# Kernel tuning notes

Hardware: AMD Instinct MI355X
Metric: run time of the kernel (lower is better)

The kernel has to match this reference:

```python
import jax, jax.numpy as jnp
import numpy as np

HC = 128   # hidden_channels
H = 8      # num_heads
D = HC // H  # projected_channels per head
N = 50000
M = 400000


def setup_inputs() -> dict:
    key = jax.random.key(0)
    ks = jax.random.split(key, 9)
    s = 1.0 / np.sqrt(HC)
    return {
        "query": jax.random.normal(ks[0], (N, HC), jnp.float32),
        "key": jax.random.normal(ks[1], (N, HC), jnp.float32),
        "query_index": jax.random.randint(ks[2], (M,), 0, N),
        "key_index": jax.random.randint(ks[3], (M,), 0, N),
        "paired_repr": jax.random.normal(ks[4], (M, HC), jnp.float32),
        "Wq": jax.random.uniform(ks[5], (HC, D * H), jnp.float32, -s, s),
        "Wkv": jax.random.uniform(ks[6], (HC, 2 * D * H), jnp.float32, -s, s),
        "Wb": jax.random.uniform(ks[7], (HC, 2 * D * H), jnp.float32, -s, s),
        "Wo": jax.random.uniform(ks[8], (D * H, HC), jnp.float32, -s, s),
    }


def reference(query, key, query_index, key_index, paired_repr, Wq, Wkv, Wb, Wo):
    n = query.shape[0]
    m = paired_repr.shape[0]
    # projections
    q = (query @ Wq).reshape(n, D, H)
    kv = key @ Wkv                              # (N, 2*D*H)
    k = kv[:, : D * H].reshape(n, D, H)
    v = kv[:, D * H :].reshape(n, D, H)
    # gather per interaction
    q_e = q[query_index]                        # (M, D, H)
    k_e = k[key_index]
    v_e = v[key_index]
    b = paired_repr @ Wb                        # (M, 2*D*H)
    bias_mul = b[:, : D * H].reshape(m, D, H)
    bias_add = b[:, D * H :].reshape(m, D, H)
    # bias-modulated dot-product logits per head
    logit = jnp.sum(q_e * (k_e * (1.0 + bias_mul) + bias_add), axis=1)  # (M, H)
    # segment softmax over query_index groups
    seg_max = jax.ops.segment_max(logit, query_index, num_segments=n)
    ex = jnp.exp(logit - seg_max[query_index])
    denom = jax.ops.segment_sum(ex, query_index, num_segments=n)
    attn = ex / denom[query_index]              # (M, H)
    # scatter-add weighted values
    agg = jax.ops.segment_sum(attn[:, None, :] * v_e, query_index, num_segments=n)  # (N, D, H)
    result = agg.reshape(n, D * H) @ Wo         # (N, HC)
    return result, logit
```

## Files before the change

### kernel.cpp

```cpp
#include <hip/hip_runtime.h>


#define HC 128
#define NH 8
#define ND 16

typedef __attribute__((ext_vector_type(8))) short bf16x8;
typedef __attribute__((ext_vector_type(4))) float f32x4;
typedef __attribute__((ext_vector_type(4))) unsigned int u32x4;

static __device__ __forceinline__ unsigned short f2bf(float f) {
  unsigned u = __float_as_uint(f);
  unsigned r = 0x7fffu + ((u >> 16) & 1u);
  return (unsigned short)((u + r) >> 16);
}
static __device__ __forceinline__ float bf2f(unsigned short h) {
  return __uint_as_float(((unsigned)h) << 16);
}

__global__ __launch_bounds__(256) void convert_wb_kernel(
    const float* __restrict__ Wb, unsigned short* __restrict__ WbTp) {
  int idx = blockIdx.x * 256 + threadIdx.x;
  int kt = idx >> 13, j = (idx >> 5) & 255, kk = idx & 31;
  WbTp[idx] = f2bf(Wb[(kt * 32 + kk) * 256 + j]);
}

__global__ __launch_bounds__(256) void count_kernel(const int* __restrict__ qidx,
                                                    int* __restrict__ cnt, int M) {
  int m = blockIdx.x * 256 + threadIdx.x;
  if (m < M) atomicAdd(&cnt[qidx[m]], 1);
}

__global__ __launch_bounds__(1024) void scan_kernel(int* __restrict__ cnt,
                                                    int* __restrict__ off, int N) {
  __shared__ int partial[1024];
  const int tid = threadIdx.x;
  const int K = (N + 1023) / 1024;
  const int lo = tid * K;
  int s = 0;
  for (int i = 0; i < K; ++i) {
    int idx = lo + i;
    if (idx < N) s += cnt[idx];
  }
  partial[tid] = s;
  __syncthreads();
  for (int d = 1; d < 1024; d <<= 1) {
    int t = (tid >= d) ? partial[tid - d] : 0;
    __syncthreads();
    partial[tid] += t;
    __syncthreads();
  }
  int run = partial[tid] - s;
  for (int i = 0; i < K; ++i) {
    int idx = lo + i;
    if (idx < N) {
      off[idx] = run;
      run += cnt[idx];
      cnt[idx] = 0;
    }
  }
  if (tid == 1023) off[N] = run;
}

__global__ __launch_bounds__(256) void fill_kernel(const int* __restrict__ qidx,
                                                   int* __restrict__ cursor,
                                                   const int* __restrict__ off,
                                                   int* __restrict__ el, int M) {
  int m = blockIdx.x * 256 + threadIdx.x;
  if (m < M) {
    int qi = qidx[m];
    int pos = atomicAdd(&cursor[qi], 1);
    el[off[qi] + pos] = m;
  }
}

__global__ __launch_bounds__(256) void proj_kernel(
    const float* __restrict__ query, const float* __restrict__ key,
    const float* __restrict__ Wq, const float* __restrict__ Wkv,
    float* __restrict__ qp, float* __restrict__ kp, float* __restrict__ vp, int N) {
  __shared__ float q_lds[16][HC];
  __shared__ float k_lds[16][HC];
  const int tid = threadIdx.x;
  const int base = blockIdx.x * 16;
  for (int i = tid; i < 16 * HC; i += 256) {
    int e = i >> 7, c = i & 127;
    int node = base + e;
    float qv = 0.f, kv = 0.f;
    if (node < N) {
      qv = query[(size_t)node * HC + c];
      kv = key[(size_t)node * HC + c];
    }
    q_lds[e][c] = qv;
    k_lds[e][c] = kv;
  }
  __syncthreads();
  {
    int j = tid & 127, e0 = tid >> 7;
    float acc[8] = {0.f, 0.f, 0.f, 0.f, 0.f, 0.f, 0.f, 0.f};
    for (int c = 0; c < HC; ++c) {
      float w = Wq[c * 128 + j];
#pragma unroll
      for (int r = 0; r < 8; ++r) acc[r] += q_lds[e0 + 2 * r][c] * w;
    }
#pragma unroll
    for (int r = 0; r < 8; ++r) {
      int node = base + e0 + 2 * r;
      if (node < N) qp[(size_t)node * 128 + j] = acc[r];
    }
  }
  {
    float acc[16];
#pragma unroll
    for (int e = 0; e < 16; ++e) acc[e] = 0.f;
    for (int c = 0; c < HC; ++c) {
      float w = Wkv[c * 256 + tid];
#pragma unroll
      for (int e = 0; e < 16; ++e) acc[e] += k_lds[e][c] * w;
    }
    float* dst = (tid < 128) ? kp : vp;
    int j = tid & 127;
#pragma unroll
    for (int e = 0; e < 16; ++e) {
      int node = base + e;
      if (node < N) dst[(size_t)node * 128 + j] = acc[e];
    }
  }
}

#define BLS 264
__global__ __launch_bounds__(256) void edge_logit_mfma(
    const float* __restrict__ pr, const unsigned short* __restrict__ WbTp,
    const float* __restrict__ qp, const float* __restrict__ kp,
    const int* __restrict__ qidx, const int* __restrict__ kidx,
    float* __restrict__ out_logit, int M) {
  __shared__ unsigned char lds[64 * BLS * 2];
  const int tid = threadIdx.x;
  const int base = blockIdx.x * 64;

#pragma unroll
  for (int i = 0; i < 4; ++i) {
    int q = tid + 256 * i;
    int row = q >> 4, cr = q & 15;
    int m = base + row;
    float4 p0 = {0.f, 0.f, 0.f, 0.f}, p1 = p0;
    if (m < M) {
      const float4* src = (const float4*)(pr + (size_t)m * HC + cr * 8);
      p0 = src[0];
      p1 = src[1];
    }
    unsigned v0 = (unsigned)f2bf(p0.x) | ((unsigned)f2bf(p0.y) << 16);
    unsigned v1 = (unsigned)f2bf(p0.z) | ((unsigned)f2bf(p0.w) << 16);
    unsigned v2 = (unsigned)f2bf(p1.x) | ((unsigned)f2bf(p1.y) << 16);
    unsigned v3 = (unsigned)f2bf(p1.z) | ((unsigned)f2bf(p1.w) << 16);
    u32x4 pk = {v0, v1, v2, v3};
    int byte = row * 256 + ((cr * 16) ^ ((row & 7) << 4));
    *(u32x4*)(lds + byte) = pk;
  }
  __syncthreads();

  const int lane = tid & 63, w = tid >> 6;
  const int arow = w * 16 + (lane & 15);
  bf16x8 a[4];
#pragma unroll
  for (int kt = 0; kt < 4; ++kt) {
    int byte = arow * 256 + ((kt * 64 + ((lane >> 4) * 16)) ^ ((arow & 7) << 4));
    a[kt] = *(const bf16x8*)(lds + byte);
  }
  __syncthreads();

  f32x4 acc[16];
#pragma unroll
  for (int n = 0; n < 16; ++n) acc[n] = (f32x4){0.f, 0.f, 0.f, 0.f};
#pragma unroll
  for (int kt = 0; kt < 4; ++kt) {
#pragma unroll
    for (int n = 0; n < 16; ++n) {
      bf16x8 b = *(const bf16x8*)(WbTp + kt * 8192 + (n * 16 + (lane & 15)) * 32 +
                                  (lane >> 4) * 8);
      acc[n] = __builtin_amdgcn_mfma_f32_16x16x32_bf16(a[kt], b, acc[n], 0, 0, 0);
    }
  }

  unsigned short* bl = (unsigned short*)lds;
  {
    int col = (lane & 15);
    int r0 = w * 16 + (lane >> 4) * 4;
#pragma unroll
    for (int n = 0; n < 16; ++n) {
#pragma unroll
      for (int r = 0; r < 4; ++r) bl[(r0 + r) * BLS + n * 16 + col] = f2bf(acc[n][r]);
    }
  }
  __syncthreads();

#pragma unroll
  for (int rep = 0; rep < 2; ++rep) {
    int unit = rep * 256 + tid;
    int e = unit >> 3, h = unit & 7;
    int m = base + e;
    if (m < M) {
      int qi = qidx[m], ki = kidx[m];
      const float* qrow = qp + (size_t)qi * HC;
      const float* krow = kp + (size_t)ki * HC;
      float s = 0.f;
#pragma unroll
      for (int d = 0; d < ND; ++d) {
        int c = d * 8 + h;
        float bm = bf2f(bl[e * BLS + c]);
        float ba = bf2f(bl[e * BLS + c + 128]);
        s += qrow[c] * (krow[c] * (1.f + bm) + ba);
      }
      out_logit[(size_t)m * 8 + h] = s;
    }
  }
}

__global__ __launch_bounds__(128) void node_agg_kernel(
    const float* __restrict__ vp, const float* __restrict__ logit,
    const int* __restrict__ kidx, const int* __restrict__ off,
    const int* __restrict__ el, float* __restrict__ agg, int N) {
  const int n = blockIdx.x;
  const int c = threadIdx.x;
  const int h = c & 7;
  const int s = off[n], e = off[n + 1];
  float mx = -1e30f;
  for (int i = s; i < e; ++i) {
    int m = el[i];
    mx = fmaxf(mx, logit[(size_t)m * 8 + h]);
  }
  float acc = 0.f, dsum = 0.f;
  for (int i = s; i < e; ++i) {
    int m = el[i];
    float ex = __expf(logit[(size_t)m * 8 + h] - mx);
    acc += ex * vp[(size_t)kidx[m] * HC + c];
    dsum += ex;
  }
  agg[(size_t)n * HC + c] = (e > s) ? acc / dsum : 0.f;
}

__global__ __launch_bounds__(256) void out_kernel(
    const float* __restrict__ agg, const float* __restrict__ Wo,
    float* __restrict__ out, int N) {
  __shared__ float a_lds[16][HC];
  const int tid = threadIdx.x;
  const int base = blockIdx.x * 16;
  for (int i = tid; i < 16 * HC; i += 256) {
    int e = i >> 7, c = i & 127;
    int node = base + e;
    a_lds[e][c] = (node < N) ? agg[(size_t)node * 128 + c] : 0.f;
  }
  __syncthreads();
  int j = tid & 127, e0 = tid >> 7;
  float acc[8] = {0.f, 0.f, 0.f, 0.f, 0.f, 0.f, 0.f, 0.f};
  for (int c = 0; c < HC; ++c) {
    float w = Wo[c * 128 + j];
#pragma unroll
    for (int r = 0; r < 8; ++r) acc[r] += a_lds[e0 + 2 * r][c] * w;
  }
#pragma unroll
  for (int r = 0; r < 8; ++r) {
    int node = base + e0 + 2 * r;
    if (node < N) out[(size_t)node * 128 + j] = acc[r];
  }
}

extern "C" void kernel_launch(void* const* d_in, const int* in_sizes, int n_in,
                              void* d_out, int out_size, void* d_ws, size_t ws_size,
                              hipStream_t stream) {
  const float* query = (const float*)d_in[0];
  const float* key   = (const float*)d_in[1];
  const int*   qidx  = (const int*)d_in[2];
  const int*   kidx  = (const int*)d_in[3];
  const float* pr    = (const float*)d_in[4];
  const float* Wq    = (const float*)d_in[5];
  const float* Wkv   = (const float*)d_in[6];
  const float* Wb    = (const float*)d_in[7];
  const float* Wo    = (const float*)d_in[8];

  const int N = in_sizes[0] / HC;
  const int M = in_sizes[2];

  float* out_result = (float*)d_out;
  float* out_logit  = (float*)d_out + (size_t)N * HC;

  float* qp  = (float*)d_ws;
  float* kp  = qp + (size_t)N * HC;
  float* vp  = kp + (size_t)N * HC;
  float* agg = vp + (size_t)N * HC;
  unsigned short* WbTp = (unsigned short*)(agg + (size_t)N * HC);
  int* cnt = (int*)(WbTp + 4 * 256 * 32);
  int* off = cnt + N;
  int* el  = off + (N + 1);

  hipMemsetAsync(cnt, 0, (size_t)N * sizeof(int), stream);
  count_kernel<<<(M + 255) / 256, 256, 0, stream>>>(qidx, cnt, M);
  scan_kernel<<<1, 1024, 0, stream>>>(cnt, off, N);
  convert_wb_kernel<<<128, 256, 0, stream>>>(Wb, WbTp);
  proj_kernel<<<(N + 15) / 16, 256, 0, stream>>>(query, key, Wq, Wkv, qp, kp, vp, N);
  edge_logit_mfma<<<(M + 63) / 64, 256, 0, stream>>>(pr, WbTp, qp, kp, qidx, kidx,
                                                     out_logit, M);
  fill_kernel<<<(M + 255) / 256, 256, 0, stream>>>(qidx, cnt, off, el, M);
  node_agg_kernel<<<N, 128, 0, stream>>>(vp, out_logit, kidx, off, el, agg, N);
  out_kernel<<<(N + 15) / 16, 256, 0, stream>>>(agg, Wo, out_result, N);
}
```

Baseline: 925.1 us.

## Move projections and output GEMM to bf16 MFMA and use online-softmax aggregation

Replaces the scalar FP32 projection and output GEMMs with bf16 MFMA kernels, using pre-converted packed weights. Stores q/k/v and the aggregate in bf16 to halve gather bandwidth. Rewrites edge logits so each wave reduces one edge's heads with shuffles. Node aggregation now runs one wave per node with a single-pass online softmax, reading precomputed (edge, key) pairs from the CSR list so kidx is no longer looked up per edge. Lower precision in the intermediates adds rounding error.

```diff
diff --git a/kernel.cpp b/kernel.cpp
--- a/kernel.cpp
+++ b/kernel.cpp
@@ -3,7 +3,6 @@
 
 #define HC 128
 #define NH 8
-#define ND 16
 
 typedef __attribute__((ext_vector_type(8))) short bf16x8;
 typedef __attribute__((ext_vector_type(4))) float f32x4;
@@ -17,12 +16,24 @@
 static __device__ __forceinline__ float bf2f(unsigned short h) {
   return __uint_as_float(((unsigned)h) << 16);
 }
-
-__global__ __launch_bounds__(256) void convert_wb_kernel(
-    const float* __restrict__ Wb, unsigned short* __restrict__ WbTp) {
+static __device__ __forceinline__ float bflo(unsigned w) { return __uint_as_float(w << 16); }
+static __device__ __forceinline__ float bfhi(unsigned w) { return __uint_as_float(w & 0xffff0000u); }
+
+__global__ __launch_bounds__(256) void convert_w_kernel(
+    const float* __restrict__ Wq, const float* __restrict__ Wkv,
+    const float* __restrict__ Wb, const float* __restrict__ Wo,
+    unsigned short* __restrict__ P) {
   int idx = blockIdx.x * 256 + threadIdx.x;
-  int kt = idx >> 13, j = (idx >> 5) & 255, kk = idx & 31;
-  WbTp[idx] = f2bf(Wb[(kt * 32 + kk) * 256 + j]);
+  const float* W;
+  int cols, local;
+  if (idx < 16384) { W = Wq; cols = 128; local = idx; }
+  else if (idx < 49152) { W = Wkv; cols = 256; local = idx - 16384; }
+  else if (idx < 81920) { W = Wb; cols = 256; local = idx - 49152; }
+  else { W = Wo; cols = 128; local = idx - 81920; }
+  int kt = local / (cols * 32);
+  int j = (local / 32) % cols;
+  int kk = local & 31;
+  P[idx] = f2bf(W[(kt * 32 + kk) * cols + j]);
 }
 
 __global__ __launch_bounds__(256) void count_kernel(const int* __restrict__ qidx,
@@ -63,102 +74,160 @@
 }
 
 __global__ __launch_bounds__(256) void fill_kernel(const int* __restrict__ qidx,
+                                                   const int* __restrict__ kidx,
                                                    int* __restrict__ cursor,
                                                    const int* __restrict__ off,
-                                                   int* __restrict__ el, int M) {
+                                                   int2* __restrict__ el2, int M) {
   int m = blockIdx.x * 256 + threadIdx.x;
   if (m < M) {
     int qi = qidx[m];
     int pos = atomicAdd(&cursor[qi], 1);
-    el[off[qi] + pos] = m;
-  }
-}
-
-__global__ __launch_bounds__(256) void proj_kernel(
+    int2 v; v.x = m; v.y = kidx[m];
+    el2[off[qi] + pos] = v;
+  }
+}
+
+__global__ __launch_bounds__(256) void proj_mfma(
     const float* __restrict__ query, const float* __restrict__ key,
-    const float* __restrict__ Wq, const float* __restrict__ Wkv,
-    float* __restrict__ qp, float* __restrict__ kp, float* __restrict__ vp, int N) {
-  __shared__ float q_lds[16][HC];
-  __shared__ float k_lds[16][HC];
+    const unsigned short* __restrict__ WqP, const unsigned short* __restrict__ WkvP,
+    unsigned short* __restrict__ qpb, unsigned short* __restrict__ kpb,
+    unsigned short* __restrict__ vpb, int N) {
+  __shared__ unsigned char lds[32768];
   const int tid = threadIdx.x;
-  const int base = blockIdx.x * 16;
-  for (int i = tid; i < 16 * HC; i += 256) {
-    int e = i >> 7, c = i & 127;
-    int node = base + e;
-    float qv = 0.f, kv = 0.f;
+  const int base = blockIdx.x * 64;
+  const int lane = tid & 63, w = tid >> 6;
+
+#pragma unroll
+  for (int i = 0; i < 4; ++i) {
+    int q = tid + 256 * i;
+    int row = q >> 4, cr = q & 15;
+    int node = base + row;
+    float4 a0 = {0.f,0.f,0.f,0.f}, a1 = a0, b0 = a0, b1 = a0;
     if (node < N) {
-      qv = query[(size_t)node * HC + c];
-      kv = key[(size_t)node * HC + c];
-    }
-    q_lds[e][c] = qv;
-    k_lds[e][c] = kv;
-  }
-  __syncthreads();
+      const float4* sq = (const float4*)(query + (size_t)node * HC + cr * 8);
+      const float4* sk = (const float4*)(key + (size_t)node * HC + cr * 8);
+      a0 = sq[0]; a1 = sq[1]; b0 = sk[0]; b1 = sk[1];
+    }
+    int byte = row * 256 + ((cr << 4) ^ ((row & 7) << 4));
+    u32x4 pa = {(unsigned)f2bf(a0.x) | ((unsigned)f2bf(a0.y) << 16),
+                (unsigned)f2bf(a0.z) | ((unsigned)f2bf(a0.w) << 16),
+                (unsigned)f2bf(a1.x) | ((unsigned)f2bf(a1.y) << 16),
+                (unsigned)f2bf(a1.z) | ((unsigned)f2bf(a1.w) << 16)};
+    u32x4 pb = {(unsigned)f2bf(b0.x) | ((unsigned)f2bf(b0.y) << 16),
+                (unsigned)f2bf(b0.z) | ((unsigned)f2bf(b0.w) << 16),
+                (unsigned)f2bf(b1.x) | ((unsigned)f2bf(b1.y) << 16),
+                (unsigned)f2bf(b1.z) | ((unsigned)f2bf(b1.w) << 16)};
+    *(u32x4*)(lds + byte) = pa;
+    *(u32x4*)(lds + 16384 + byte) = pb;
+  }
+  __syncthreads();
+
+  const int arow = w * 16 + (lane & 15);
+  bf16x8 aq[4], ak[4];
+#pragma unroll
+  for (int kt = 0; kt < 4; ++kt) {
+    int byte = arow * 256 + ((kt * 64 + ((lane >> 4) * 16)) ^ ((arow & 7) << 4));
+    aq[kt] = *(const bf16x8*)(lds + byte);
+    ak[kt] = *(const bf16x8*)(lds + 16384 + byte);
+  }
+  __syncthreads();
+
+  unsigned short* stg = (unsigned short*)lds;
+
   {
-    int j = tid & 127, e0 = tid >> 7;
-    float acc[8] = {0.f, 0.f, 0.f, 0.f, 0.f, 0.f, 0.f, 0.f};
-    for (int c = 0; c < HC; ++c) {
-      float w = Wq[c * 128 + j];
-#pragma unroll
-      for (int r = 0; r < 8; ++r) acc[r] += q_lds[e0 + 2 * r][c] * w;
-    }
-#pragma unroll
-    for (int r = 0; r < 8; ++r) {
-      int node = base + e0 + 2 * r;
-      if (node < N) qp[(size_t)node * 128 + j] = acc[r];
-    }
-  }
+    f32x4 acc[8];
+#pragma unroll
+    for (int n = 0; n < 8; ++n) acc[n] = (f32x4){0.f,0.f,0.f,0.f};
+#pragma unroll
+    for (int kt = 0; kt < 4; ++kt)
+#pragma unroll
+      for (int n = 0; n < 8; ++n) {
+        bf16x8 b = *(const bf16x8*)(WqP + kt * 4096 + (n * 16 + (lane & 15)) * 32 + (lane >> 4) * 8);
+        acc[n] = __builtin_amdgcn_mfma_f32_16x16x32_bf16(aq[kt], b, acc[n], 0, 0, 0);
+      }
+    int lc = lane & 15, r0 = w * 16 + (lane >> 4) * 4;
+#pragma unroll
+    for (int n = 0; n < 8; ++n)
+#pragma unroll
+      for (int r = 0; r < 4; ++r) {
+        int row = r0 + r, col = n * 16 + lc;
+        int byte = row * 256 + ((((col >> 3) ^ (row & 7)) << 4)) + (col & 7) * 2;
+        *(unsigned short*)((unsigned char*)stg + byte) = f2bf(acc[n][r]);
+      }
+#pragma unroll
+    for (int it = 0; it < 4; ++it) {
+      int q = it * 64 + lane;
+      int row = w * 16 + (q >> 4), ch = q & 15;
+      int node = base + row;
+      u32x4 v = *(const u32x4*)(lds + row * 256 + ((ch ^ (row & 7)) << 4));
+      if (node < N) *(u32x4*)(qpb + (size_t)node * HC + ch * 8) = v;
+    }
+  }
+
   {
-    float acc[16];
-#pragma unroll
-    for (int e = 0; e < 16; ++e) acc[e] = 0.f;
-    for (int c = 0; c < HC; ++c) {
-      float w = Wkv[c * 256 + tid];
-#pragma unroll
-      for (int e = 0; e < 16; ++e) acc[e] += k_lds[e][c] * w;
-    }
-    float* dst = (tid < 128) ? kp : vp;
-    int j = tid & 127;
-#pragma unroll
-    for (int e = 0; e < 16; ++e) {
-      int node = base + e;
-      if (node < N) dst[(size_t)node * 128 + j] = acc[e];
+    f32x4 acc[16];
+#pragma unroll
+    for (int n = 0; n < 16; ++n) acc[n] = (f32x4){0.f,0.f,0.f,0.f};
+#pragma unroll
+    for (int kt = 0; kt < 4; ++kt)
+#pragma unroll
+      for (int n = 0; n < 16; ++n) {
+        bf16x8 b = *(const bf16x8*)(WkvP + kt * 8192 + (n * 16 + (lane & 15)) * 32 + (lane >> 4) * 8);
+        acc[n] = __builtin_amdgcn_mfma_f32_16x16x32_bf16(ak[kt], b, acc[n], 0, 0, 0);
+      }
+    int lc = lane & 15, r0 = w * 16 + (lane >> 4) * 4;
+#pragma unroll
+    for (int half = 0; half < 2; ++half) {
+#pragma unroll
+      for (int n = 0; n < 8; ++n)
+#pragma unroll
+        for (int r = 0; r < 4; ++r) {
+          int row = r0 + r, col = n * 16 + lc;
+          int byte = row * 256 + ((((col >> 3) ^ (row & 7)) << 4)) + (col & 7) * 2;
+          *(unsigned short*)((unsigned char*)stg + byte) = f2bf(acc[half * 8 + n][r]);
+        }
+      unsigned short* dst = half ? vpb : kpb;
+#pragma unroll
+      for (int it = 0; it < 4; ++it) {
+        int q = it * 64 + lane;
+        int row = w * 16 + (q >> 4), ch = q & 15;
+        int node = base + row;
+        u32x4 v = *(const u32x4*)(lds + row * 256 + ((ch ^ (row & 7)) << 4));
+        if (node < N) *(u32x4*)(dst + (size_t)node * HC + ch * 8) = v;
+      }
     }
   }
 }
 
 #define BLS 264
 __global__ __launch_bounds__(256) void edge_logit_mfma(
-    const float* __restrict__ pr, const unsigned short* __restrict__ WbTp,
-    const float* __restrict__ qp, const float* __restrict__ kp,
+    const float* __restrict__ pr, const unsigned short* __restrict__ WbP,
+    const unsigned short* __restrict__ qpb, const unsigned short* __restrict__ kpb,
     const int* __restrict__ qidx, const int* __restrict__ kidx,
     float* __restrict__ out_logit, int M) {
   __shared__ unsigned char lds[64 * BLS * 2];
   const int tid = threadIdx.x;
   const int base = blockIdx.x * 64;
+  const int lane = tid & 63, w = tid >> 6;
 
 #pragma unroll
   for (int i = 0; i < 4; ++i) {
     int q = tid + 256 * i;
     int row = q >> 4, cr = q & 15;
     int m = base + row;
-    float4 p0 = {0.f, 0.f, 0.f, 0.f}, p1 = p0;
+    float4 p0 = {0.f,0.f,0.f,0.f}, p1 = p0;
     if (m < M) {
       const float4* src = (const float4*)(pr + (size_t)m * HC + cr * 8);
-      p0 = src[0];
-      p1 = src[1];
-    }
-    unsigned v0 = (unsigned)f2bf(p0.x) | ((unsigned)f2bf(p0.y) << 16);
-    unsigned v1 = (unsigned)f2bf(p0.z) | ((unsigned)f2bf(p0.w) << 16);
-    unsigned v2 = (unsigned)f2bf(p1.x) | ((unsigned)f2bf(p1.y) << 16);
-    unsigned v3 = (unsigned)f2bf(p1.z) | ((unsigned)f2bf(p1.w) << 16);
-    u32x4 pk = {v0, v1, v2, v3};
-    int byte = row * 256 + ((cr * 16) ^ ((row & 7) << 4));
-    *(u32x4*)(lds + byte) = pk;
-  }
-  __syncthreads();
-
-  const int lane = tid & 63, w = tid >> 6;
+      p0 = src[0]; p1 = src[1];
+    }
+    u32x4 pk = {(unsigned)f2bf(p0.x) | ((unsigned)f2bf(p0.y) << 16),
+                (unsigned)f2bf(p0.z) | ((unsigned)f2bf(p0.w) << 16),
+                (unsigned)f2bf(p1.x) | ((unsigned)f2bf(p1.y) << 16),
+                (unsigned)f2bf(p1.z) | ((unsigned)f2bf(p1.w) << 16)};
+    *(u32x4*)(lds + row * 256 + ((cr << 4) ^ ((row & 7) << 4))) = pk;
+  }
+  __syncthreads();
+
   const int arow = w * 16 + (lane & 15);
   bf16x8 a[4];
 #pragma unroll
@@ -170,97 +239,136 @@
 
   f32x4 acc[16];
 #pragma unroll
-  for (int n = 0; n < 16; ++n) acc[n] = (f32x4){0.f, 0.f, 0.f, 0.f};
-#pragma unroll
-  for (int kt = 0; kt < 4; ++kt) {
+  for (int n = 0; n < 16; ++n) acc[n] = (f32x4){0.f,0.f,0.f,0.f};
+#pragma unroll
+  for (int kt = 0; kt < 4; ++kt)
 #pragma unroll
     for (int n = 0; n < 16; ++n) {
-      bf16x8 b = *(const bf16x8*)(WbTp + kt * 8192 + (n * 16 + (lane & 15)) * 32 +
-                                  (lane >> 4) * 8);
+      bf16x8 b = *(const bf16x8*)(WbP + kt * 8192 + (n * 16 + (lane & 15)) * 32 + (lane >> 4) * 8);
       acc[n] = __builtin_amdgcn_mfma_f32_16x16x32_bf16(a[kt], b, acc[n], 0, 0, 0);
     }
-  }
 
   unsigned short* bl = (unsigned short*)lds;
   {
-    int col = (lane & 15);
-    int r0 = w * 16 + (lane >> 4) * 4;
-#pragma unroll
-    for (int n = 0; n < 16; ++n) {
+    int col = lane & 15, r0 = w * 16 + (lane >> 4) * 4;
+#pragma unroll
+    for (int n = 0; n < 16; ++n)
 #pragma unroll
       for (int r = 0; r < 4; ++r) bl[(r0 + r) * BLS + n * 16 + col] = f2bf(acc[n][r]);
-    }
-  }
-  __syncthreads();
-
-#pragma unroll
-  for (int rep = 0; rep < 2; ++rep) {
-    int unit = rep * 256 + tid;
-    int e = unit >> 3, h = unit & 7;
+  }
+  __syncthreads();
+
+#pragma unroll 2
+  for (int i = 0; i < 16; ++i) {
+    int e = w * 16 + i;
     int m = base + e;
     if (m < M) {
       int qi = qidx[m], ki = kidx[m];
-      const float* qrow = qp + (size_t)qi * HC;
-      const float* krow = kp + (size_t)ki * HC;
-      float s = 0.f;
-#pragma unroll
-      for (int d = 0; d < ND; ++d) {
-        int c = d * 8 + h;
-        float bm = bf2f(bl[e * BLS + c]);
-        float ba = bf2f(bl[e * BLS + c + 128]);
-        s += qrow[c] * (krow[c] * (1.f + bm) + ba);
-      }
-      out_logit[(size_t)m * 8 + h] = s;
-    }
-  }
-}
-
-__global__ __launch_bounds__(128) void node_agg_kernel(
-    const float* __restrict__ vp, const float* __restrict__ logit,
-    const int* __restrict__ kidx, const int* __restrict__ off,
-    const int* __restrict__ el, float* __restrict__ agg, int N) {
-  const int n = blockIdx.x;
-  const int c = threadIdx.x;
-  const int h = c & 7;
+      unsigned qw = *(const unsigned*)(qpb + (size_t)qi * HC + 2 * lane);
+      unsigned kw = *(const unsigned*)(kpb + (size_t)ki * HC + 2 * lane);
+      unsigned bmw = *(const unsigned*)(bl + e * BLS + 2 * lane);
+      unsigned baw = *(const unsigned*)(bl + e * BLS + 128 + 2 * lane);
+      float p0 = bflo(qw) * (bflo(kw) * (1.f + bflo(bmw)) + bflo(baw));
+      float p1 = bfhi(qw) * (bfhi(kw) * (1.f + bfhi(bmw)) + bfhi(baw));
+#pragma unroll
+      for (int msk = 4; msk <= 32; msk <<= 1) {
+        p0 += __shfl_xor(p0, msk);
+        p1 += __shfl_xor(p1, msk);
+      }
+      if (lane < 4) {
+        float2 v; v.x = p0; v.y = p1;
+        *(float2*)(out_logit + (size_t)m * NH + 2 * lane) = v;
+      }
+    }
+  }
+}
+
+__global__ __launch_bounds__(256) void node_agg_kernel(
+    const unsigned short* __restrict__ vpb, const float* __restrict__ logit,
+    const int* __restrict__ off, const int2* __restrict__ el2,
+    unsigned short* __restrict__ aggb, int N) {
+  const int lane = threadIdx.x & 63, w = threadIdx.x >> 6;
+  const int n = blockIdx.x * 4 + w;
+  if (n >= N) return;
   const int s = off[n], e = off[n + 1];
-  float mx = -1e30f;
+  const int t = lane & 3;
+  float mx0 = -1e30f, mx1 = -1e30f, d0 = 0.f, d1 = 0.f, a0 = 0.f, a1 = 0.f;
   for (int i = s; i < e; ++i) {
-    int m = el[i];
-    mx = fmaxf(mx, logit[(size_t)m * 8 + h]);
-  }
-  float acc = 0.f, dsum = 0.f;
-  for (int i = s; i < e; ++i) {
-    int m = el[i];
-    float ex = __expf(logit[(size_t)m * 8 + h] - mx);
-    acc += ex * vp[(size_t)kidx[m] * HC + c];
-    dsum += ex;
-  }
-  agg[(size_t)n * HC + c] = (e > s) ? acc / dsum : 0.f;
-}
-
-__global__ __launch_bounds__(256) void out_kernel(
-    const float* __restrict__ agg, const float* __restrict__ Wo,
+    int2 me = el2[i];
+    float2 lg = *(const float2*)(logit + (size_t)me.x * NH + 2 * t);
+    unsigned vw = *(const unsigned*)(vpb + (size_t)me.y * HC + 2 * lane);
+    float nm0 = fmaxf(mx0, lg.x), nm1 = fmaxf(mx1, lg.y);
+    float s0 = __expf(mx0 - nm0), s1 = __expf(mx1 - nm1);
+    float e0 = __expf(lg.x - nm0), e1 = __expf(lg.y - nm1);
+    a0 = a0 * s0 + e0 * bflo(vw);
+    a1 = a1 * s1 + e1 * bfhi(vw);
+    d0 = d0 * s0 + e0;
+    d1 = d1 * s1 + e1;
+    mx0 = nm0; mx1 = nm1;
+  }
+  float r0 = (e > s) ? a0 / d0 : 0.f;
+  float r1 = (e > s) ? a1 / d1 : 0.f;
+  unsigned pk = (unsigned)f2bf(r0) | ((unsigned)f2bf(r1) << 16);
+  *(unsigned*)(aggb + (size_t)n * HC + 2 * lane) = pk;
+}
+
+__global__ __launch_bounds__(256) void out_mfma(
+    const unsigned short* __restrict__ aggb, const unsigned short* __restrict__ WoP,
     float* __restrict__ out, int N) {
-  __shared__ float a_lds[16][HC];
+  __shared__ unsigned char lds[16384 + 32768];
   const int tid = threadIdx.x;
-  const int base = blockIdx.x * 16;
-  for (int i = tid; i < 16 * HC; i += 256) {
-    int e = i >> 7, c = i & 127;
-    int node = base + e;
-    a_lds[e][c] = (node < N) ? agg[(size_t)node * 128 + c] : 0.f;
-  }
-  __syncthreads();
-  int j = tid & 127, e0 = tid >> 7;
-  float acc[8] = {0.f, 0.f, 0.f, 0.f, 0.f, 0.f, 0.f, 0.f};
-  for (int c = 0; c < HC; ++c) {
-    float w = Wo[c * 128 + j];
-#pragma unroll
-    for (int r = 0; r < 8; ++r) acc[r] += a_lds[e0 + 2 * r][c] * w;
-  }
-#pragma unroll
-  for (int r = 0; r < 8; ++r) {
-    int node = base + e0 + 2 * r;
-    if (node < N) out[(size_t)node * 128 + j] = acc[r];
+  const int base = blockIdx.x * 64;
+  const int lane = tid & 63, w = tid >> 6;
+
+#pragma unroll
+  for (int i = 0; i < 4; ++i) {
+    int q = tid + 256 * i;
+    int row = q >> 4, cr = q & 15;
+    int node = base + row;
+    u32x4 v = {0u,0u,0u,0u};
+    if (node < N) v = *(const u32x4*)(aggb + (size_t)node * HC + cr * 8);
+    *(u32x4*)(lds + row * 256 + ((cr << 4) ^ ((row & 7) << 4))) = v;
+  }
+  __syncthreads();
+
+  const int arow = w * 16 + (lane & 15);
+  bf16x8 a[4];
+#pragma unroll
+  for (int kt = 0; kt < 4; ++kt) {
+    int byte = arow * 256 + ((kt * 64 + ((lane >> 4) * 16)) ^ ((arow & 7) << 4));
+    a[kt] = *(const bf16x8*)(lds + byte);
+  }
+
+  f32x4 acc[8];
+#pragma unroll
+  for (int n = 0; n < 8; ++n) acc[n] = (f32x4){0.f,0.f,0.f,0.f};
+#pragma unroll
+  for (int kt = 0; kt < 4; ++kt)
+#pragma unroll
+    for (int n = 0; n < 8; ++n) {
+      bf16x8 b = *(const bf16x8*)(WoP + kt * 4096 + (n * 16 + (lane & 15)) * 32 + (lane >> 4) * 8);
+      acc[n] = __builtin_amdgcn_mfma_f32_16x16x32_bf16(a[kt], b, acc[n], 0, 0, 0);
+    }
+
+  float* fs = (float*)(lds + 16384);
+  {
+    int lc = lane & 15, r0 = w * 16 + (lane >> 4) * 4;
+#pragma unroll
+    for (int n = 0; n < 8; ++n)
+#pragma unroll
+      for (int r = 0; r < 4; ++r) {
+        int row = r0 + r, col = n * 16 + lc;
+        int byte = row * 512 + ((((col >> 2) ^ (row & 7)) << 4)) + (col & 3) * 4;
+        *(float*)((unsigned char*)fs + byte) = acc[n][r];
+      }
+  }
+#pragma unroll
+  for (int it = 0; it < 8; ++it) {
+    int q = it * 64 + lane;
+    int row = w * 16 + (q >> 5), ch = q & 31;
+    int node = base + row;
+    f32x4 v = *(const f32x4*)((unsigned char*)fs + row * 512 + ((ch ^ (row & 7)) << 4));
+    if (node < N) *(f32x4*)(out + (size_t)node * HC + ch * 4) = v;
   }
 }
 
@@ -283,23 +391,27 @@
   float* out_result = (float*)d_out;
   float* out_logit  = (float*)d_out + (size_t)N * HC;
 
-  float* qp  = (float*)d_ws;
-  float* kp  = qp + (size_t)N * HC;
-  float* vp  = kp + (size_t)N * HC;
-  float* agg = vp + (size_t)N * HC;
-  unsigned short* WbTp = (unsigned short*)(agg + (size_t)N * HC);
-  int* cnt = (int*)(WbTp + 4 * 256 * 32);
-  int* off = cnt + N;
-  int* el  = off + (N + 1);
+  unsigned short* qpb  = (unsigned short*)d_ws;
+  unsigned short* kpb  = qpb + (size_t)N * HC;
+  unsigned short* vpb  = kpb + (size_t)N * HC;
+  unsigned short* aggb = vpb + (size_t)N * HC;
+  unsigned short* WP   = aggb + (size_t)N * HC;
+  unsigned short* WqP  = WP;
+  unsigned short* WkvP = WP + 16384;
+  unsigned short* WbP  = WP + 49152;
+  unsigned short* WoP  = WP + 81920;
+  int*  cnt = (int*)(WP + 98304);
+  int*  off = cnt + N;
+  int2* el2 = (int2*)(off + ((N + 4) & ~3));
 
   hipMemsetAsync(cnt, 0, (size_t)N * sizeof(int), stream);
   count_kernel<<<(M + 255) / 256, 256, 0, stream>>>(qidx, cnt, M);
   scan_kernel<<<1, 1024, 0, stream>>>(cnt, off, N);
-  convert_wb_kernel<<<128, 256, 0, stream>>>(Wb, WbTp);
-  proj_kernel<<<(N + 15) / 16, 256, 0, stream>>>(query, key, Wq, Wkv, qp, kp, vp, N);
-  edge_logit_mfma<<<(M + 63) / 64, 256, 0, stream>>>(pr, WbTp, qp, kp, qidx, kidx,
+  fill_kernel<<<(M + 255) / 256, 256, 0, stream>>>(qidx, kidx, cnt, off, el2, M);
+  convert_w_kernel<<<384, 256, 0, stream>>>(Wq, Wkv, Wb, Wo, WP);
+  proj_mfma<<<(N + 63) / 64, 256, 0, stream>>>(query, key, WqP, WkvP, qpb, kpb, vpb, N);
+  edge_logit_mfma<<<(M + 63) / 64, 256, 0, stream>>>(pr, WbP, qpb, kpb, qidx, kidx,
                                                      out_logit, M);
-  fill_kernel<<<(M + 255) / 256, 256, 0, stream>>>(qidx, cnt, off, el, M);
-  node_agg_kernel<<<N, 128, 0, stream>>>(vp, out_logit, kidx, off, el, agg, N);
-  out_kernel<<<(N + 15) / 16, 256, 0, stream>>>(agg, Wo, out_result, N);
-}
+  node_agg_kernel<<<(N + 3) / 4, 256, 0, stream>>>(vpb, out_logit, off, el2, aggb, N);
+  out_mfma<<<(N + 63) / 64, 256, 0, stream>>>(aggb, WoP, out_result, N);
+}
```

Result: faster. 788.8 us (-14.7%).
